# Optimization experiments

Measured on AMD Instinct MI355X. Metric: run time of the kernel, lower is better.

## Reference

```python
import jax, jax.numpy as jnp
import numpy as np

G = 64          # number of global tokens (first G positions are global)
NUM_HEADS = 16
WINDOW = 512    # attention_window (one-sided w = 256)


def _chunk(x, w):
    # x: [BH, S, D] -> overlapping chunks of size 2w with overlap w
    BH, S, D = x.shape
    f = x.reshape(BH, S // w, w, D)
    return jnp.concatenate([f[:, :-1], f[:, 1:]], axis=2)  # [BH, S//w-1, 2w, D]


def _mask_invalid(x, w):
    # x: [B, S, H, 2w+1]; -inf at out-of-sequence window positions
    B, S, H, W = x.shape
    m = jnp.flip(jnp.tril(jnp.ones((w, w + 1), x.dtype)), axis=0)
    m = jnp.pad(m, ((0, S - w), (0, W - w - 1)))
    m = m + jnp.flip(m, axis=(0, 1))
    return jnp.where((m > 0)[None, :, None, :], -jnp.inf, x)


def _sliding_qk(q, k, w):
    # q, k: [B, S, H, D] -> banded scores [B, S, H, 2w+1]
    B, S, H, D = q.shape
    C = S // w - 1
    qf = q.transpose(0, 2, 1, 3).reshape(B * H, S, D)
    kf = k.transpose(0, 2, 1, 3).reshape(B * H, S, D)
    s = jnp.einsum('bcxd,bcyd->bcxy', _chunk(qf, w), _chunk(kf, w))  # [BH,C,2w,2w]
    diag = jnp.pad(s, ((0, 0), (0, 0), (0, 1), (0, 0))).transpose(0, 1, 3, 2)  # [BH,C,2w,2w+1]
    up = jnp.concatenate([diag[:, :, :w, :w + 1], diag[:, -1:, w:, :w + 1]], axis=1)
    z = jnp.zeros((B * H, 1, w, w), diag.dtype)
    low = jnp.concatenate([z, diag[:, :, -(w + 1):-1, w + 1:]], axis=1)
    first = jnp.concatenate([jnp.roll(diag, shift=(1, w), axis=(2, 3))[:, :, :w, :w], z], axis=1)
    low = jnp.where(jnp.arange(C + 1)[None, :, None, None] < 1, first, low)
    full = jnp.concatenate([low, up], axis=-1).reshape(B, H, S, 2 * w + 1).transpose(0, 2, 1, 3)
    return _mask_invalid(full, w)


def _sliding_pv(probs, v, w):
    # probs: [B, S, H, 2w+1], v: [B, S, H, D] -> [B, S, H, D]
    B, S, H, _ = probs.shape
    D = v.shape[-1]
    nc = S // w
    p = probs.transpose(0, 2, 1, 3).reshape(B * H, nc, w, 2 * w + 1)
    vf = v.transpose(0, 2, 1, 3).reshape(B * H, S, D)
    pv = jnp.pad(vf, ((0, 0), (w, w), (0, 0)), constant_values=-1.0)
    idx = jnp.arange(nc)[:, None] * w + jnp.arange(3 * w)[None, :]
    cv = pv[:, idx]  # [BH, nc, 3w, D]
    # pad-and-diagonalize the banded probs into [w, 3w]
    pd = jnp.pad(p, ((0, 0), (0, 0), (0, 0), (0, w + 1)))
    pd = pd.reshape(B * H, nc, w * (3 * w + 2))[:, :, :-w]
    pd = pd.reshape(B * H, nc, w, 3 * w + 1)[:, :, :, :-1]  # [BH,nc,w,3w]
    out = jnp.einsum('bcwd,bcdh->bcwh', pd, cv)
    return out.reshape(B, H, S, D).transpose(0, 2, 1, 3)


def _forward(hidden_states, attention_mask, Wq, bq, Wk, bk, Wv, bv,
             Wqg, bqg, Wkg, bkg, Wvg, bvg, is_index_masked, is_index_global_attn):
    B, S, E = hidden_states.shape
    H = NUM_HEADS
    D = E // H
    w = WINDOW // 2
    q = (hidden_states @ Wq + bq) / jnp.sqrt(jnp.float32(D))
    k = hidden_states @ Wk + bk
    v = hidden_states @ Wv + bv
    q4 = q.reshape(B, S, H, D)
    k4 = k.reshape(B, S, H, D)
    v4 = v.reshape(B, S, H, D)
    local = _sliding_qk(q4, k4, w)                         # [B,S,H,2w+1]
    diag_mask = _sliding_qk(jnp.ones_like(attention_mask), attention_mask, w)  # [B,S,1,2w+1]
    local = local + diag_mask
    # global key columns (first G tokens global) prepended to the band
    g_scores = jnp.einsum('bshd,bghd->bshg', q4, k4[:, :G])
    scores = jnp.concatenate([g_scores, local], axis=-1)   # [B,S,H,G+2w+1]
    probs = jax.nn.softmax(scores, axis=-1)
    probs = jnp.where(is_index_masked[:, :, None, None], 0.0, probs)
    out_g = jnp.einsum('bshg,bghd->bshd', probs[..., :G], v4[:, :G])
    out_l = _sliding_pv(probs[..., G:], v4, w)
    attn_output = (out_g + out_l).reshape(B, S, E)
    # global tokens attend to the full sequence with the *_global projections
    qg = ((hidden_states[:, :G] @ Wqg + bqg) / jnp.sqrt(jnp.float32(D))).reshape(B, G, H, D).transpose(0, 2, 1, 3)
    kg = (hidden_states @ Wkg + bkg).reshape(B, S, H, D).transpose(0, 2, 1, 3)
    vg = (hidden_states @ Wvg + bvg).reshape(B, S, H, D).transpose(0, 2, 1, 3)
    gs = jnp.einsum('bhgd,bhsd->bhgs', qg, kg)             # [B,H,G,S]
    gs = jnp.where(is_index_masked[:, None, None, :], -10000.0, gs)
    gp = jax.nn.softmax(gs, axis=-1)
    go = jnp.einsum('bhgs,bhsd->bhgd', gp, vg).transpose(0, 2, 1, 3).reshape(B, G, E)
    attn_output = attn_output.at[:, :G].set(go)            # scatter global rows
    probs = jnp.where(is_index_global_attn[:, :, None, None], 0.0, probs)
    return attn_output, probs, gp


def setup_inputs() -> dict:
    key = jax.random.key(0)
    B, S, E = 2, 4096, 1024
    ks = jax.random.split(key, 8)
    std = 0.02
    d = lambda k: std * jax.random.normal(k, (E, E), jnp.float32)
    zb = jnp.zeros((E,), jnp.float32)
    return {
        'hidden_states': jax.random.normal(ks[0], (B, S, E), jnp.float32),
        'attention_mask': jnp.zeros((B, S, 1, 1), jnp.float32),
        'Wq': d(ks[1]), 'bq': zb, 'Wk': d(ks[2]), 'bk': zb, 'Wv': d(ks[3]), 'bv': zb,
        'Wqg': d(ks[4]), 'bqg': zb, 'Wkg': d(ks[5]), 'bkg': zb, 'Wvg': d(ks[6]), 'bvg': zb,
        'is_index_masked': jnp.zeros((B, S), bool),
        'is_index_global_attn': jnp.broadcast_to(jnp.arange(S)[None, :] < G, (B, S)),
        'is_global_attn': 1,
    }


def reference(hidden_states, attention_mask, Wq, bq, Wk, bk, Wv, bv,
              Wqg, bqg, Wkg, bkg, Wvg, bvg,
              is_index_masked, is_index_global_attn, is_global_attn):
    # is_global_attn is statically 1 (global path always taken)
    return _forward(hidden_states, attention_mask, Wq, bq, Wk, bk, Wv, bv,
                    Wqg, bqg, Wkg, bkg, Wvg, bvg, is_index_masked, is_index_global_attn)
```

## Files before the change

kernel.cpp:

```cpp
#include <hip/hip_runtime.h>
#include <hip/hip_bf16.h>
#include <cstdint>
#include <cstddef>

typedef short s16x8 __attribute__((ext_vector_type(8)));
typedef float f32x4 __attribute__((ext_vector_type(4)));

#define DEV static __device__ __forceinline__

DEV unsigned short f2bf(float x){
  union { float f; unsigned int u; } v; v.f = x;
  unsigned int u = v.u;
  return (unsigned short)((u + 0x7FFFu + ((u >> 16) & 1u)) >> 16);
}
DEV float bf2f(unsigned short b){
  union { unsigned int u; float f; } v; v.u = ((unsigned int)b) << 16;
  return v.f;
}

DEV void gld16(unsigned short* lds, const unsigned short* g){
  __builtin_amdgcn_global_load_lds(
      (const __attribute__((address_space(1))) void*)g,
      (__attribute__((address_space(3))) void*)lds, 16, 0, 0);
}

__global__ __launch_bounds__(256) void cast_x(const float* __restrict__ X,
                                              unsigned short* __restrict__ out){
  int i = (blockIdx.x*256 + threadIdx.x)*4;
  float4 v = *(const float4*)(X + i);
  ushort4 r;
  r.x = f2bf(v.x); r.y = f2bf(v.y); r.z = f2bf(v.z); r.w = f2bf(v.w);
  *(ushort4*)(out + i) = r;
}

__global__ __launch_bounds__(256) void xg_gather(const float* __restrict__ X,
                                                 unsigned short* __restrict__ Xg){
  int idx = blockIdx.x*256 + threadIdx.x;
  int row = idx >> 10, c = idx & 1023;
  int b = row >> 6, g = row & 63;
  Xg[idx] = f2bf(X[(size_t)(b*4096 + g)*1024 + c]);
}

__global__ __launch_bounds__(256) void bias_cat_k(
    const float* bq, const float* bk, const float* bv,
    const float* bkg, const float* bvg, const float* bqg,
    float* __restrict__ bc, float* __restrict__ bqg_o){
  int i = blockIdx.x*256 + threadIdx.x;
  if (i < 5120){
    int slot = i >> 10, c = i & 1023;
    const float* s = (slot==0)?bq:(slot==1)?bk:(slot==2)?bv:(slot==3)?bkg:bvg;
    bc[i] = s[c];
  } else {
    bqg_o[i-5120] = bqg[i-5120];
  }
}

struct WSrc { const float* p[6]; };

__global__ __launch_bounds__(256) void wt_transpose(WSrc srcs,
    unsigned short* __restrict__ Wtcat, unsigned short* __restrict__ Wtqg){
  __shared__ float t[64*66];
  int bi = blockIdx.x;
  int widx = bi >> 8;
  int tile = bi & 255;
  int tn = tile & 15, tk = tile >> 4;
  int k0 = tk*64, n0 = tn*64;
  const float* W = srcs.p[widx];
  int tid = threadIdx.x;
  for (int it=0; it<8; ++it){
    int flat = it*256 + tid;
    int r = flat >> 5, ch = flat & 31;
    *(float2*)&t[r*66 + ch*2] = *(const float2*)(W + (size_t)(k0+r)*1024 + n0 + ch*2);
  }
  __syncthreads();
  unsigned short* dst = (widx==3) ? Wtqg
                      : Wtcat + (size_t)((widx<3)?widx:widx-1)*1048576;
  for (int it=0; it<16; ++it){
    int flat = it*256 + tid;
    int i = flat >> 6, j = flat & 63;
    dst[(size_t)(n0+i)*1024 + k0 + j] = f2bf(t[j*66 + i]);
  }
}

__global__ __launch_bounds__(256) void gemm_bt(
    const unsigned short* __restrict__ A, const unsigned short* __restrict__ Bt,
    const float* __restrict__ bias, unsigned short* __restrict__ C,
    int Astr, int Bstr, int Cstr, int scale_cols)
{
  __shared__ unsigned short lA[128*64];
  __shared__ unsigned short lB[128*64];
  int tid = threadIdx.x, lane = tid & 63, wv = tid >> 6;
  int wm = wv >> 1, wn = wv & 1;
  int lane15 = lane & 15, kh = (lane >> 4) << 3;
  int m0 = blockIdx.y*128, n0 = blockIdx.x*128;
  f32x4 acc[4][4];
  for (int i=0;i<4;i++) for (int j=0;j<4;j++) acc[i][j] = (f32x4){0.f,0.f,0.f,0.f};
  for (int k0 = 0; k0 < 1024; k0 += 64){
#pragma unroll
    for (int it = 0; it < 4; ++it){
      int chunk = it*256 + tid;
      int r = chunk >> 3, ch = chunk & 7;
      int co = ((ch ^ (r & 7)) << 3);
      gld16(&lA[chunk*8], A  + (size_t)(m0+r)*Astr + k0 + co);
      gld16(&lB[chunk*8], Bt + (size_t)(n0+r)*Bstr + k0 + co);
    }
    __syncthreads();
#pragma unroll
    for (int ks = 0; ks < 2; ++ks){
      s16x8 af[4], bfr[4];
#pragma unroll
      for (int i=0;i<4;i++){
        int row = wm*64 + i*16 + lane15;
        af[i] = *(const s16x8*)&lA[(row<<6) + ((ks*32 + kh) ^ ((row&7)<<3))];
      }
#pragma unroll
      for (int j=0;j<4;j++){
        int row = wn*64 + j*16 + lane15;
        bfr[j] = *(const s16x8*)&lB[(row<<6) + ((ks*32 + kh) ^ ((row&7)<<3))];
      }
#pragma unroll
      for (int i=0;i<4;i++)
#pragma unroll
        for (int j=0;j<4;j++)
          acc[i][j] = __builtin_amdgcn_mfma_f32_16x16x32_bf16(af[i], bfr[j], acc[i][j], 0,0,0);
    }
    __syncthreads();
  }
  for (int i=0;i<4;i++){
    int mb = m0 + wm*64 + i*16 + ((lane>>4)<<2);
    for (int j=0;j<4;j++){
      int n = n0 + wn*64 + j*16 + lane15;
      float bb = bias[n];
      float sc = (n < scale_cols) ? 0.125f : 1.0f;
#pragma unroll
      for (int r=0;r<4;r++)
        C[(size_t)(mb+r)*Cstr + n] = f2bf((acc[i][j][r] + bb)*sc);
    }
  }
}

__global__ __launch_bounds__(256) void vt_transpose(
    const unsigned short* __restrict__ proj, unsigned short* __restrict__ dst,
    int coloff){
  __shared__ unsigned short t[64*72];
  int bi = blockIdx.x;
  int sc = bi & 63, h = (bi>>6) & 15, b = bi >> 10;
  int s0 = sc*64;
  int tid = threadIdx.x;
  for (int it=0; it<2; ++it){
    int flat = it*256 + tid;
    int r = flat >> 3, ch = flat & 7;
    *(int4*)&t[r*72 + ch*8] =
      *(const int4*)(proj + (size_t)(b*4096+s0+r)*5120 + coloff + h*64 + ch*8);
  }
  __syncthreads();
  for (int it=0; it<2; ++it){
    int flat = it*256 + tid;
    int d = flat & 63, ch = flat >> 6;
    unsigned short tmp[8];
#pragma unroll
    for (int j=0;j<8;j++) tmp[j] = t[(ch*8+j)*72 + d];
    *(int4*)(dst + ((size_t)(b*16+h)*64 + d)*4096 + s0 + ch*8) = *(int4*)tmp;
  }
}

#define SSTR 612
__global__ __launch_bounds__(256) void sliding_attn(
    const unsigned short* __restrict__ proj,
    const unsigned short* __restrict__ vt,
    const float* __restrict__ amask,
    const unsigned char* __restrict__ maskb,
    float* __restrict__ probs,
    float* __restrict__ attn)
{
  __shared__ float sS[16*SSTR];
  __shared__ float srs[16];
  int bi = (blockIdx.x & 7)*1024 + (blockIdx.x >> 3);
  int ti = bi & 255, h = (bi>>8) & 15, b = bi >> 12;
  int t = ti*16;
  int chk = t >> 8;
  int qu = (chk < 15) ? chk*256 : 3584;
  int ql = (chk >= 1) ? chk*256 : 256;
  int tid = threadIdx.x, lane = tid & 63, wv = tid >> 6;
  int lane15 = lane & 15, kh = (lane >> 4) << 3;
  int rbase = (lane>>4)<<2;

  s16x8 aq0, aq1, ak0a, ak0b, ak1a, ak1b;
  {
    int qrow = t + lane15;
    const unsigned short* qp = proj + (size_t)(b*4096+qrow)*5120 + h*64 + kh;
    aq0 = *(const s16x8*)qp;  aq1 = *(const s16x8*)(qp + 32);
    const unsigned short* kp0 = proj + (size_t)(b*4096+qrow)*5120 + 1024 + h*64 + kh;
    ak0a = *(const s16x8*)kp0; ak0b = *(const s16x8*)(kp0 + 32);
    int krow = t - 1 + lane15; if (krow < 0) krow = 0;
    const unsigned short* kp1 = proj + (size_t)(b*4096+krow)*5120 + 1024 + h*64 + kh;
    ak1a = *(const s16x8*)kp1; ak1b = *(const s16x8*)(kp1 + 32);
  }

  {
    int ct0 = (wv==0)?0:(wv==1)?10:(wv==2)?19:28;
    int ntt = (wv==0)?10:9;
    s16x8 B0[5], B1[5];
#pragma unroll
    for (int bb=0; bb<2; ++bb){
      int base = ct0 + bb*5;
      int cnt = ct0 + ntt - base; if (cnt > 5) cnt = 5;
#pragma unroll
      for (int j=0;j<5;++j){
        if (j < cnt){
          int ct = base + j;
          int col = ct*16 + lane15;
          int brow, roff;
          if (ct < 4){        brow = col;               roff = 1024; }
          else if (ct < 20){  brow = ql + 1 + col - 64; roff = 0;
                              if (brow > 4095) brow = 4095; }
          else {              brow = qu + col - 320;    roff = 0; }
          const unsigned short* bp = proj + (size_t)(b*4096+brow)*5120 + roff + h*64 + kh;
          B0[j] = *(const s16x8*)bp;
          B1[j] = *(const s16x8*)(bp + 32);
        }
      }
#pragma unroll
      for (int j=0;j<5;++j){
        if (j < cnt){
          int ct = base + j;
          s16x8 A0 = (ct<4) ? aq0 : (ct<20) ? ak1a : ak0a;
          s16x8 A1 = (ct<4) ? aq1 : (ct<20) ? ak1b : ak0b;
          f32x4 acc = (f32x4){0.f,0.f,0.f,0.f};
          acc = __builtin_amdgcn_mfma_f32_16x16x32_bf16(A0, B0[j], acc, 0,0,0);
          acc = __builtin_amdgcn_mfma_f32_16x16x32_bf16(A1, B1[j], acc, 0,0,0);
          int col = ct*16 + lane15;
          if (col <= 576){
            int sk = (ct >= 4);
#pragma unroll
            for (int r=0;r<4;r++){
              int row = rbase + r;
              sS[row*SSTR + col + (sk ? row : 0)] = acc[r];
            }
          }
        }
      }
    }
  }
  __syncthreads();

  {
    int r0 = wv*4;
    float low_add[4], up_add[4];
#pragma unroll
    for (int rr=0;rr<4;rr++){
      int s = t + r0 + rr;
      low_add[rr] = (s >= 1) ? amask[b*4096 + s - 1] : 0.f;
      up_add[rr]  = amask[b*4096 + s];
    }
    float ereg[4][10];
    float m4[4] = {-1e30f,-1e30f,-1e30f,-1e30f};
#pragma unroll
    for (int i=0;i<10;i++){
      int c = lane + i*64;
      bool inr = (c < 577);
      bool isup = (c >= 320), islow = (c >= 64) & !isup;
      int jup = c - 320, jlow = c - 64;
#pragma unroll
      for (int rr=0;rr<4;rr++){
        int r = r0 + rr;
        float v = -1e30f;
        if (inr){
          v = sS[r*SSTR + c + ((c>=64) ? r : 0)];
          int ii = (t + r) & 255;
          if (isup){
            bool valid = !((chk==15) & (jup >= 256 - ii));
            v = valid ? v + up_add[rr] : -1e30f;
          } else if (islow){
            bool valid = !((chk==0) & (jlow < 256 - ii));
            v = valid ? ((jlow==255) ? 0.f : v + low_add[rr]) : -1e30f;
          }
        }
        ereg[rr][i] = v;
        m4[rr] = fmaxf(m4[rr], v);
      }
    }
#pragma unroll
    for (int o=32;o;o>>=1){
#pragma unroll
      for (int rr=0;rr<4;rr++) m4[rr] = fmaxf(m4[rr], __shfl_xor(m4[rr], o));
    }
    float sum4[4] = {0.f,0.f,0.f,0.f};
#pragma unroll
    for (int i=0;i<10;i++){
      int c = lane + i*64;
      if (c < 577){
#pragma unroll
        for (int rr=0;rr<4;rr++){
          int r = r0 + rr;
          float e = __expf(ereg[rr][i] - m4[rr]);
          ereg[rr][i] = e;
          sum4[rr] += e;
          ((unsigned short*)&sS[r*SSTR])[c + ((c>=64) ? r : 0)] = f2bf(e);
        }
      }
    }
#pragma unroll
    for (int o=32;o;o>>=1){
#pragma unroll
      for (int rr=0;rr<4;rr++) sum4[rr] += __shfl_xor(sum4[rr], o);
    }
#pragma unroll
    for (int rr=0;rr<4;rr++){
      int r = r0 + rr, s = t + r;
      float rs = 1.f / sum4[rr];
      float mz = maskb[b*4096 + s] ? 0.f : 1.f;
      float pz = (s < 64) ? 0.f : mz;
      float* prow = probs + ((size_t)(b*4096+s)*16 + h)*577;
#pragma unroll
      for (int i=0;i<10;i++){
        int c = lane + i*64;
        if (c < 577) prow[c] = ereg[rr][i] * rs * pz;
      }
      if (lane < 31){
        int zc = (lane < r) ? 64 + lane : 577 + lane;
        ((unsigned short*)&sS[r*SSTR])[zc] = 0;
      }
      if (lane == 0) srs[r] = rs * mz;
    }
  }
  __syncthreads();

  int dcol = wv*16 + lane15;
  const unsigned short* vtb = vt + ((size_t)(b*16+h)*64 + dcol)*4096;
  const unsigned short* prow16 = (const unsigned short*)(sS + (size_t)lane15*SSTR);
  s16x8 vb[8];
#pragma unroll
  for (int kc=0; kc<8; ++kc){
    int kk = kc*32 + kh;
    int key = (kk < 64) ? kk : (t - 320 + kk);
    key = key < 0 ? 0 : (key > 4088 ? 4088 : key);
    vb[kc] = *(const s16x8*)(vtb + key);
  }
  f32x4 oacc = (f32x4){0.f,0.f,0.f,0.f};
#pragma unroll
  for (int kc = 0; kc < 19; ++kc){
    s16x8 ap = *(const s16x8*)(prow16 + kc*32 + kh);
    oacc = __builtin_amdgcn_mfma_f32_16x16x32_bf16(ap, vb[kc & 7], oacc, 0,0,0);
    int kn = kc + 8;
    if (kn < 19){
      int kk = kn*32 + kh;
      int key = (kk < 64) ? kk : (t - 320 + kk);
      key = key < 0 ? 0 : (key > 4088 ? 4088 : key);
      vb[kn & 7] = *(const s16x8*)(vtb + key);
    }
  }
#pragma unroll
  for (int r=0;r<4;r++)
    attn[(size_t)(b*4096 + t + rbase + r)*1024 + h*64 + dcol] = oacc[r] * srs[rbase + r];
}

__global__ __launch_bounds__(256) void gs_a2(
    const unsigned short* __restrict__ qg,
    const unsigned short* __restrict__ proj,
    const unsigned char* __restrict__ maskb,
    float* __restrict__ gp)
{
  __shared__ unsigned short sQ[64*68];
  int bi = blockIdx.x;
  int sc = bi & 15, h = (bi>>4) & 15, b = bi >> 8;
  int tid = threadIdx.x, lane = tid & 63, wv = tid >> 6;
  int lane15 = lane & 15, kh = (lane >> 4) << 3;
#pragma unroll
  for (int it=0; it<2; ++it){
    int flat = it*256 + tid;
    int g = flat >> 3, ch = (flat & 7) << 3;
    *(s16x8*)&sQ[g*68 + ch] = *(const s16x8*)(qg + (size_t)(b*64+g)*1024 + h*64 + ch);
  }
  __syncthreads();
  s16x8 a[4][2];
#pragma unroll
  for (int gt=0; gt<4; ++gt)
#pragma unroll
    for (int ks=0; ks<2; ++ks)
      a[gt][ks] = *(const s16x8*)&sQ[(gt*16+lane15)*68 + ks*32 + kh];
  int s0 = sc*256 + wv*64;
  float* gpb_ = gp + (size_t)(b*16+h)*64*4096;
#pragma unroll
  for (int st=0; st<4; ++st){
    int s = s0 + st*16 + lane15;
    const unsigned short* kp = proj + (size_t)(b*4096+s)*5120 + 3072 + h*64 + kh;
    s16x8 b0 = *(const s16x8*)kp;
    s16x8 b1 = *(const s16x8*)(kp + 32);
    bool msk = maskb[b*4096 + s] != 0;
    f32x4 acc[4];
#pragma unroll
    for (int gt=0; gt<4; ++gt){
      acc[gt] = (f32x4){0.f,0.f,0.f,0.f};
      acc[gt] = __builtin_amdgcn_mfma_f32_16x16x32_bf16(a[gt][0], b0, acc[gt], 0,0,0);
      acc[gt] = __builtin_amdgcn_mfma_f32_16x16x32_bf16(a[gt][1], b1, acc[gt], 0,0,0);
    }
#pragma unroll
    for (int gt=0; gt<4; ++gt){
#pragma unroll
      for (int r=0;r<4;r++){
        int g = gt*16 + (lane>>4)*4 + r;
        gpb_[(size_t)g*4096 + s] = msk ? -10000.f : acc[gt][r];
      }
    }
  }
}

__global__ __launch_bounds__(256) void gs_norm(float* __restrict__ gp,
                                               unsigned short* __restrict__ gpb){
  __shared__ float red[8];
  int bi = blockIdx.x;
  float* row = gp + (size_t)bi*4096;
  int tid = threadIdx.x, lane = tid & 63, wv = tid >> 6;
  float v[16];
  float m = -1e30f;
#pragma unroll
  for (int i=0;i<16;i++){
    v[i] = row[tid + i*256];
    m = fmaxf(m, v[i]);
  }
#pragma unroll
  for (int o=32;o;o>>=1) m = fmaxf(m, __shfl_xor(m, o));
  if (!lane) red[wv] = m;
  __syncthreads();
  m = fmaxf(fmaxf(red[0],red[1]), fmaxf(red[2],red[3]));
  float s = 0.f;
#pragma unroll
  for (int i=0;i<16;i++){
    float e = __expf(v[i] - m);
    v[i] = e;
    s += e;
  }
#pragma unroll
  for (int o=32;o;o>>=1) s += __shfl_xor(s, o);
  if (!lane) red[4+wv] = s;
  __syncthreads();
  s = red[4]+red[5]+red[6]+red[7];
  float rs = 1.f / s;
#pragma unroll
  for (int i=0;i<16;i++){
    float p = v[i] * rs;
    row[tid + i*256] = p;
    gpb[(size_t)bi*4096 + tid + i*256] = f2bf(p);
  }
}

__global__ __launch_bounds__(256) void go_mfma(
    const unsigned short* __restrict__ gpb,
    const unsigned short* __restrict__ vgt,
    float* __restrict__ gop)
{
  int bi = blockIdx.x;
  int kc = bi & 7, bh = bi >> 3;
  int tid = threadIdx.x, lane = tid & 63, wv = tid >> 6;
  int lane15 = lane & 15, kh = (lane >> 4) << 3;
  const unsigned short* arow = gpb + ((size_t)bh*64 + wv*16 + lane15)*4096 + kh;
  const unsigned short* bbase = vgt + (size_t)bh*64*4096 + kh;
  f32x4 acc[4];
#pragma unroll
  for (int j=0;j<4;j++) acc[j] = (f32x4){0.f,0.f,0.f,0.f};
  for (int ks = 0; ks < 16; ++ks){
    int k = kc*512 + ks*32;
    s16x8 a = *(const s16x8*)(arow + k);
#pragma unroll
    for (int j=0;j<4;j++){
      s16x8 bv = *(const s16x8*)(bbase + (size_t)(j*16 + lane15)*4096 + k);
      acc[j] = __builtin_amdgcn_mfma_f32_16x16x32_bf16(a, bv, acc[j], 0,0,0);
    }
  }
  int rq = (lane >> 4) << 2;
  float* o = gop + ((size_t)bh*8 + kc)*4096;
#pragma unroll
  for (int j=0;j<4;j++)
#pragma unroll
    for (int r=0;r<4;r++)
      o[(wv*16 + rq + r)*64 + j*16 + lane15] = acc[j][r];
}

__global__ __launch_bounds__(256) void reduce_go2(
    const float* __restrict__ gop, float* __restrict__ attn){
  int flat = blockIdx.x*256 + threadIdx.x;
  int gd = flat & 4095, bh = flat >> 12;
  int b = bh >> 4, h = bh & 15;
  int g = gd >> 6, d = gd & 63;
  const float* p = gop + (size_t)bh*8*4096 + gd;
  float sum = 0.f;
#pragma unroll
  for (int c=0; c<8; ++c) sum += p[c*4096];
  attn[(size_t)(b*4096 + g)*1024 + h*64 + d] = sum;
}

extern "C" void kernel_launch(void* const* d_in, const int* in_sizes, int n_in,
                              void* d_out, int out_size, void* d_ws, size_t ws_size,
                              hipStream_t stream)
{
  const float* X     = (const float*)d_in[0];
  const float* amask = (const float*)d_in[1];
  const float* Wq  = (const float*)d_in[2];  const float* bq  = (const float*)d_in[3];
  const float* Wk  = (const float*)d_in[4];  const float* bk  = (const float*)d_in[5];
  const float* Wv  = (const float*)d_in[6];  const float* bv  = (const float*)d_in[7];
  const float* Wqg = (const float*)d_in[8];  const float* bqg = (const float*)d_in[9];
  const float* Wkg = (const float*)d_in[10]; const float* bkg = (const float*)d_in[11];
  const float* Wvg = (const float*)d_in[12]; const float* bvg = (const float*)d_in[13];
  const unsigned char* imask = (const unsigned char*)d_in[14];
  (void)in_sizes; (void)n_in; (void)out_size;

  const size_t XBF  = 0;
  const size_t XG   = 16777216;
  const size_t WT   = 17039360;
  const size_t WTQG = 27525120;
  const size_t BC   = 29622272;
  const size_t BQG  = 29642752;
  const size_t PROJ = 29646848;
  const size_t QGO  = 113532928;
  const size_t VT   = 113795072;
  const size_t NEED = 130572288;
  if (ws_size < NEED) return;

  char* ws = (char*)d_ws;
  unsigned short* Xbf   = (unsigned short*)(ws + XBF);
  unsigned short* Xg    = (unsigned short*)(ws + XG);
  unsigned short* Wtcat = (unsigned short*)(ws + WT);
  unsigned short* Wtqg  = (unsigned short*)(ws + WTQG);
  float*          bc    = (float*)(ws + BC);
  float*          bqgo  = (float*)(ws + BQG);
  unsigned short* proj  = (unsigned short*)(ws + PROJ);
  unsigned short* qgo   = (unsigned short*)(ws + QGO);
  unsigned short* vt    = (unsigned short*)(ws + VT);
  unsigned short* gpb   = (unsigned short*)(ws + XBF);
  float*          gop   = (float*)(ws + WT);

  float* attn  = (float*)d_out;
  float* probs = (float*)d_out + 8388608;
  float* gp    = (float*)d_out + 84017152;

  cast_x<<<8192, 256, 0, stream>>>(X, Xbf);
  xg_gather<<<512, 256, 0, stream>>>(X, Xg);
  bias_cat_k<<<24, 256, 0, stream>>>(bq, bk, bv, bkg, bvg, bqg, bc, bqgo);
  WSrc srcs; srcs.p[0]=Wq; srcs.p[1]=Wk; srcs.p[2]=Wv; srcs.p[3]=Wqg; srcs.p[4]=Wkg; srcs.p[5]=Wvg;
  wt_transpose<<<1536, 256, 0, stream>>>(srcs, Wtcat, Wtqg);
  gemm_bt<<<dim3(40,64), 256, 0, stream>>>(Xbf, Wtcat, bc, proj, 1024, 1024, 5120, 1024);
  gemm_bt<<<dim3(8,1),  256, 0, stream>>>(Xg, Wtqg, bqgo, qgo, 1024, 1024, 1024, 1024);
  vt_transpose<<<2048, 256, 0, stream>>>(proj, vt, 2048);
  sliding_attn<<<8192, 256, 0, stream>>>(proj, vt, amask, imask, probs, attn);
  vt_transpose<<<2048, 256, 0, stream>>>(proj, vt, 4096);
  gs_a2<<<512, 256, 0, stream>>>(qgo, proj, imask, gp);
  gs_norm<<<2048, 256, 0, stream>>>(gp, gpb);
  go_mfma<<<256, 256, 0, stream>>>(gpb, vt, gop);
  reduce_go2<<<512, 256, 0, stream>>>(gop, attn);
}
```

Before: 420.1 us.

## Use 8 waves in sliding attention and XCD-swizzle GEMM block order

The sliding-window attention kernel moves from 4 to 8 waves per block. QK column tiles are spread over 8 waves, softmax handles 2 rows per wave, and the PV product is split along K across two wave halves, with the partial sums combined through shared memory before the write. The projection GEMM switches to a 1D grid and remaps block indices so that neighbouring tiles land on the same XCD, aiming for better L2 reuse. The attention change trades a simpler loop without V prefetch, plus an extra barrier and reduction, for more waves in flight to hide latency.

```diff
diff --git a/kernel.cpp b/kernel.cpp
--- a/kernel.cpp
+++ b/kernel.cpp
@@ -85,14 +85,17 @@
 __global__ __launch_bounds__(256) void gemm_bt(
     const unsigned short* __restrict__ A, const unsigned short* __restrict__ Bt,
     const float* __restrict__ bias, unsigned short* __restrict__ C,
-    int Astr, int Bstr, int Cstr, int scale_cols)
+    int Astr, int Bstr, int Cstr, int scale_cols, int ny)
 {
   __shared__ unsigned short lA[128*64];
   __shared__ unsigned short lB[128*64];
+  int cpx = gridDim.x >> 3;
+  int bi = (blockIdx.x & 7)*cpx + (blockIdx.x >> 3);
+  int bx = bi / ny, by = bi % ny;
   int tid = threadIdx.x, lane = tid & 63, wv = tid >> 6;
   int wm = wv >> 1, wn = wv & 1;
   int lane15 = lane & 15, kh = (lane >> 4) << 3;
-  int m0 = blockIdx.y*128, n0 = blockIdx.x*128;
+  int m0 = by*128, n0 = bx*128;
   f32x4 acc[4][4];
   for (int i=0;i<4;i++) for (int j=0;j<4;j++) acc[i][j] = (f32x4){0.f,0.f,0.f,0.f};
   for (int k0 = 0; k0 < 1024; k0 += 64){
@@ -165,7 +168,7 @@
 }
 
 #define SSTR 612
-__global__ __launch_bounds__(256) void sliding_attn(
+__global__ __launch_bounds__(512) void sliding_attn(
     const unsigned short* __restrict__ proj,
     const unsigned short* __restrict__ vt,
     const float* __restrict__ amask,
@@ -185,76 +188,65 @@
   int lane15 = lane & 15, kh = (lane >> 4) << 3;
   int rbase = (lane>>4)<<2;
 
-  s16x8 aq0, aq1, ak0a, ak0b, ak1a, ak1b;
+  s16x8 aq0 = {}, aq1 = {}, ak0a = {}, ak0b = {}, ak1a = {}, ak1b = {};
   {
     int qrow = t + lane15;
-    const unsigned short* qp = proj + (size_t)(b*4096+qrow)*5120 + h*64 + kh;
-    aq0 = *(const s16x8*)qp;  aq1 = *(const s16x8*)(qp + 32);
-    const unsigned short* kp0 = proj + (size_t)(b*4096+qrow)*5120 + 1024 + h*64 + kh;
-    ak0a = *(const s16x8*)kp0; ak0b = *(const s16x8*)(kp0 + 32);
-    int krow = t - 1 + lane15; if (krow < 0) krow = 0;
-    const unsigned short* kp1 = proj + (size_t)(b*4096+krow)*5120 + 1024 + h*64 + kh;
-    ak1a = *(const s16x8*)kp1; ak1b = *(const s16x8*)(kp1 + 32);
+    if (wv == 0){
+      const unsigned short* qp = proj + (size_t)(b*4096+qrow)*5120 + h*64 + kh;
+      aq0 = *(const s16x8*)qp;  aq1 = *(const s16x8*)(qp + 32);
+    }
+    if (wv >= 4 || wv == 3){
+      const unsigned short* kp0 = proj + (size_t)(b*4096+qrow)*5120 + 1024 + h*64 + kh;
+      ak0a = *(const s16x8*)kp0; ak0b = *(const s16x8*)(kp0 + 32);
+    }
+    if (wv <= 3){
+      int krow = t - 1 + lane15; if (krow < 0) krow = 0;
+      const unsigned short* kp1 = proj + (size_t)(b*4096+krow)*5120 + 1024 + h*64 + kh;
+      ak1a = *(const s16x8*)kp1; ak1b = *(const s16x8*)(kp1 + 32);
+    }
   }
 
   {
-    int ct0 = (wv==0)?0:(wv==1)?10:(wv==2)?19:28;
-    int ntt = (wv==0)?10:9;
-    s16x8 B0[5], B1[5];
-#pragma unroll
-    for (int bb=0; bb<2; ++bb){
-      int base = ct0 + bb*5;
-      int cnt = ct0 + ntt - base; if (cnt > 5) cnt = 5;
-#pragma unroll
-      for (int j=0;j<5;++j){
-        if (j < cnt){
-          int ct = base + j;
-          int col = ct*16 + lane15;
-          int brow, roff;
-          if (ct < 4){        brow = col;               roff = 1024; }
-          else if (ct < 20){  brow = ql + 1 + col - 64; roff = 0;
-                              if (brow > 4095) brow = 4095; }
-          else {              brow = qu + col - 320;    roff = 0; }
-          const unsigned short* bp = proj + (size_t)(b*4096+brow)*5120 + roff + h*64 + kh;
-          B0[j] = *(const s16x8*)bp;
-          B1[j] = *(const s16x8*)(bp + 32);
+    int ct0 = wv*5;
+    int ctend = (ct0 + 5 > 37) ? 37 : ct0 + 5;
+    for (int ct = ct0; ct < ctend; ++ct){
+      int col = ct*16 + lane15;
+      int brow, roff;
+      if (ct < 4){        brow = col;               roff = 1024; }
+      else if (ct < 20){  brow = ql + 1 + col - 64; roff = 0;
+                          if (brow > 4095) brow = 4095; }
+      else {              brow = qu + col - 320;    roff = 0; }
+      const unsigned short* bp = proj + (size_t)(b*4096+brow)*5120 + roff + h*64 + kh;
+      s16x8 b0 = *(const s16x8*)bp;
+      s16x8 b1 = *(const s16x8*)(bp + 32);
+      s16x8 A0 = (ct<4) ? aq0 : (ct<20) ? ak1a : ak0a;
+      s16x8 A1 = (ct<4) ? aq1 : (ct<20) ? ak1b : ak0b;
+      f32x4 acc = (f32x4){0.f,0.f,0.f,0.f};
+      acc = __builtin_amdgcn_mfma_f32_16x16x32_bf16(A0, b0, acc, 0,0,0);
+      acc = __builtin_amdgcn_mfma_f32_16x16x32_bf16(A1, b1, acc, 0,0,0);
+      if (col <= 576){
+        int sk = (ct >= 4);
+#pragma unroll
+        for (int r=0;r<4;r++){
+          int row = rbase + r;
+          sS[row*SSTR + col + (sk ? row : 0)] = acc[r];
         }
       }
-#pragma unroll
-      for (int j=0;j<5;++j){
-        if (j < cnt){
-          int ct = base + j;
-          s16x8 A0 = (ct<4) ? aq0 : (ct<20) ? ak1a : ak0a;
-          s16x8 A1 = (ct<4) ? aq1 : (ct<20) ? ak1b : ak0b;
-          f32x4 acc = (f32x4){0.f,0.f,0.f,0.f};
-          acc = __builtin_amdgcn_mfma_f32_16x16x32_bf16(A0, B0[j], acc, 0,0,0);
-          acc = __builtin_amdgcn_mfma_f32_16x16x32_bf16(A1, B1[j], acc, 0,0,0);
-          int col = ct*16 + lane15;
-          if (col <= 576){
-            int sk = (ct >= 4);
-#pragma unroll
-            for (int r=0;r<4;r++){
-              int row = rbase + r;
-              sS[row*SSTR + col + (sk ? row : 0)] = acc[r];
-            }
-          }
-        }
-      }
     }
   }
   __syncthreads();
 
   {
-    int r0 = wv*4;
-    float low_add[4], up_add[4];
-#pragma unroll
-    for (int rr=0;rr<4;rr++){
+    int r0 = wv*2;
+    float low_add[2], up_add[2];
+#pragma unroll
+    for (int rr=0;rr<2;rr++){
       int s = t + r0 + rr;
       low_add[rr] = (s >= 1) ? amask[b*4096 + s - 1] : 0.f;
       up_add[rr]  = amask[b*4096 + s];
     }
-    float ereg[4][10];
-    float m4[4] = {-1e30f,-1e30f,-1e30f,-1e30f};
+    float ereg[2][10];
+    float m4[2] = {-1e30f,-1e30f};
 #pragma unroll
     for (int i=0;i<10;i++){
       int c = lane + i*64;
@@ -262,7 +254,7 @@
       bool isup = (c >= 320), islow = (c >= 64) & !isup;
       int jup = c - 320, jlow = c - 64;
 #pragma unroll
-      for (int rr=0;rr<4;rr++){
+      for (int rr=0;rr<2;rr++){
         int r = r0 + rr;
         float v = -1e30f;
         if (inr){
@@ -283,15 +275,15 @@
 #pragma unroll
     for (int o=32;o;o>>=1){
 #pragma unroll
-      for (int rr=0;rr<4;rr++) m4[rr] = fmaxf(m4[rr], __shfl_xor(m4[rr], o));
-    }
-    float sum4[4] = {0.f,0.f,0.f,0.f};
+      for (int rr=0;rr<2;rr++) m4[rr] = fmaxf(m4[rr], __shfl_xor(m4[rr], o));
+    }
+    float sum4[2] = {0.f,0.f};
 #pragma unroll
     for (int i=0;i<10;i++){
       int c = lane + i*64;
       if (c < 577){
 #pragma unroll
-        for (int rr=0;rr<4;rr++){
+        for (int rr=0;rr<2;rr++){
           int r = r0 + rr;
           float e = __expf(ereg[rr][i] - m4[rr]);
           ereg[rr][i] = e;
@@ -303,10 +295,10 @@
 #pragma unroll
     for (int o=32;o;o>>=1){
 #pragma unroll
-      for (int rr=0;rr<4;rr++) sum4[rr] += __shfl_xor(sum4[rr], o);
-    }
-#pragma unroll
-    for (int rr=0;rr<4;rr++){
+      for (int rr=0;rr<2;rr++) sum4[rr] += __shfl_xor(sum4[rr], o);
+    }
+#pragma unroll
+    for (int rr=0;rr<2;rr++){
       int r = r0 + rr, s = t + r;
       float rs = 1.f / sum4[rr];
       float mz = maskb[b*4096 + s] ? 0.f : 1.f;
@@ -326,33 +318,38 @@
   }
   __syncthreads();
 
-  int dcol = wv*16 + lane15;
+  int dg = wv & 3, khalf = wv >> 2;
+  int dcol = dg*16 + lane15;
   const unsigned short* vtb = vt + ((size_t)(b*16+h)*64 + dcol)*4096;
   const unsigned short* prow16 = (const unsigned short*)(sS + (size_t)lane15*SSTR);
-  s16x8 vb[8];
-#pragma unroll
-  for (int kc=0; kc<8; ++kc){
+  f32x4 oacc = (f32x4){0.f,0.f,0.f,0.f};
+  int kc0 = khalf*10, kcn = khalf ? 9 : 10;
+  for (int kci = 0; kci < kcn; ++kci){
+    int kc = kc0 + kci;
     int kk = kc*32 + kh;
+    s16x8 ap = *(const s16x8*)(prow16 + kk);
     int key = (kk < 64) ? kk : (t - 320 + kk);
     key = key < 0 ? 0 : (key > 4088 ? 4088 : key);
-    vb[kc] = *(const s16x8*)(vtb + key);
-  }
-  f32x4 oacc = (f32x4){0.f,0.f,0.f,0.f};
-#pragma unroll
-  for (int kc = 0; kc < 19; ++kc){
-    s16x8 ap = *(const s16x8*)(prow16 + kc*32 + kh);
-    oacc = __builtin_amdgcn_mfma_f32_16x16x32_bf16(ap, vb[kc & 7], oacc, 0,0,0);
-    int kn = kc + 8;
-    if (kn < 19){
-      int kk = kn*32 + kh;
-      int key = (kk < 64) ? kk : (t - 320 + kk);
-      key = key < 0 ? 0 : (key > 4088 ? 4088 : key);
-      vb[kn & 7] = *(const s16x8*)(vtb + key);
-    }
-  }
-#pragma unroll
-  for (int r=0;r<4;r++)
-    attn[(size_t)(b*4096 + t + rbase + r)*1024 + h*64 + dcol] = oacc[r] * srs[rbase + r];
+    s16x8 bv = *(const s16x8*)(vtb + key);
+    oacc = __builtin_amdgcn_mfma_f32_16x16x32_bf16(ap, bv, oacc, 0,0,0);
+  }
+  if (khalf == 1){
+#pragma unroll
+    for (int r=0;r<4;r++){
+      int flat = dg*256 + (rbase + r)*16 + lane15;
+      sS[(flat>>8)*SSTR + 336 + (flat & 255)] = oacc[r];
+    }
+  }
+  __syncthreads();
+  if (khalf == 0){
+#pragma unroll
+    for (int r=0;r<4;r++){
+      int flat = dg*256 + (rbase + r)*16 + lane15;
+      float part = sS[(flat>>8)*SSTR + 336 + (flat & 255)];
+      attn[(size_t)(b*4096 + t + rbase + r)*1024 + h*64 + dcol] =
+          (oacc[r] + part) * srs[rbase + r];
+    }
+  }
 }
 
 __global__ __launch_bounds__(256) void gs_a2(
@@ -539,10 +536,10 @@
   bias_cat_k<<<24, 256, 0, stream>>>(bq, bk, bv, bkg, bvg, bqg, bc, bqgo);
   WSrc srcs; srcs.p[0]=Wq; srcs.p[1]=Wk; srcs.p[2]=Wv; srcs.p[3]=Wqg; srcs.p[4]=Wkg; srcs.p[5]=Wvg;
   wt_transpose<<<1536, 256, 0, stream>>>(srcs, Wtcat, Wtqg);
-  gemm_bt<<<dim3(40,64), 256, 0, stream>>>(Xbf, Wtcat, bc, proj, 1024, 1024, 5120, 1024);
-  gemm_bt<<<dim3(8,1),  256, 0, stream>>>(Xg, Wtqg, bqgo, qgo, 1024, 1024, 1024, 1024);
+  gemm_bt<<<2560, 256, 0, stream>>>(Xbf, Wtcat, bc, proj, 1024, 1024, 5120, 1024, 64);
+  gemm_bt<<<8,    256, 0, stream>>>(Xg, Wtqg, bqgo, qgo, 1024, 1024, 1024, 1024, 1);
   vt_transpose<<<2048, 256, 0, stream>>>(proj, vt, 2048);
-  sliding_attn<<<8192, 256, 0, stream>>>(proj, vt, amask, imask, probs, attn);
+  sliding_attn<<<8192, 512, 0, stream>>>(proj, vt, amask, imask, probs, attn);
   vt_transpose<<<2048, 256, 0, stream>>>(proj, vt, 4096);
   gs_a2<<<512, 256, 0, stream>>>(qgo, proj, imask, gp);
   gs_norm<<<2048, 256, 0, stream>>>(gp, gpb);
```

Result: slower. 438.3 us (+4.3%).
